# Performance work log

Hardware: AMD Instinct MI355X
Metric: run time of the kernel (lower is better)

The kernel has to match this reference:

```python
import jax, jax.numpy as jnp
import numpy as np

D_MODEL = 1024
D_STATE = 16
EPS = 1e-5


def _layernorm(x, g, b):
    mu = x.mean(-1, keepdims=True)
    xc = x - mu
    var = (xc * xc).mean(-1, keepdims=True)
    return xc * jax.lax.rsqrt(var + EPS) * g + b


def setup_inputs() -> dict:
    key = jax.random.key(0)
    ks = jax.random.split(key, 10)
    B, L, d, n = 8, 1024, D_MODEL, D_STATE
    s = 1.0 / np.sqrt(d)
    return {
        "x": jax.random.normal(ks[0], (B, L, d), jnp.float32),
        "h_prev": jnp.zeros((B, d * n), jnp.float32),
        "ln_g": jnp.ones((d,), jnp.float32),
        "ln_b": jnp.zeros((d,), jnp.float32),
        "W_ig": jax.random.uniform(ks[1], (2 * d, d), jnp.float32, -s, s),
        "W_dt": jax.random.uniform(ks[2], (d, d), jnp.float32, -s, s),
        "b_dt": jax.random.uniform(ks[3], (d,), jnp.float32, -s, s),
        "A_log": jax.random.uniform(ks[4], (d, n), jnp.float32, -3.0, -1.0),
        "W_B": jax.random.uniform(ks[5], (n, d), jnp.float32, -s, s),
        "W_C": jax.random.uniform(ks[6], (n, d), jnp.float32, -s, s),
        "D": jnp.ones((d,), jnp.float32),
        "W_out": jax.random.uniform(ks[7], (d, d), jnp.float32, -s, s),
    }


def reference(x, h_prev, ln_g, ln_b, W_ig, W_dt, b_dt, A_log, W_B, W_C, D, W_out):
    Bsz, L, d = x.shape
    n = A_log.shape[1]
    x_norm = _layernorm(x, ln_g, ln_b)
    x_proj = jnp.einsum('bld,ed->ble', x_norm, W_ig)  # [B,L,2d]
    x_in, z = x_proj[..., :d], x_proj[..., d:]
    dt = jax.nn.softplus(jnp.einsum('bld,ed->ble', x_in, W_dt) + b_dt)  # [B,L,d]
    A = -jnp.exp(A_log)  # [d,n]
    B_t = jnp.einsum('bld,nd->bln', x_in, W_B)  # [B,L,n]
    C_t = jnp.einsum('bld,nd->bln', x_in, W_C)  # [B,L,n]
    h0 = h_prev.reshape(Bsz, d, n)

    def step(h, inp):
        dt_t, xin_t, Bt_t, Ct_t = inp  # [B,d],[B,d],[B,n],[B,n]
        dA = jnp.exp(dt_t[..., None] * A)                      # [B,d,n]
        h = dA * h + (dt_t * xin_t)[..., None] * Bt_t[:, None, :]
        y_t = (h * Ct_t[:, None, :]).sum(-1)                   # [B,d]
        return h, y_t

    xs = (jnp.swapaxes(dt, 0, 1), jnp.swapaxes(x_in, 0, 1),
          jnp.swapaxes(B_t, 0, 1), jnp.swapaxes(C_t, 0, 1))
    h_final, y = jax.lax.scan(step, h0, xs)
    y = jnp.swapaxes(y, 0, 1)  # [B,L,d]
    ssm_out = y * jax.nn.silu(z) + x_in * D
    out = jnp.einsum('bld,ed->ble', ssm_out, W_out)
    return (x + out, h_final.reshape(Bsz, -1))
```

## Files before the change

### kernel.cpp

```cpp
#include <hip/hip_runtime.h>
#include <hip/hip_bf16.h>
#include <math.h>

#define DM 1024
#define NS 16
#define BSZ 8
#define LSEQ 1024
#define MROWS (BSZ*LSEQ)
#define CH 32
#define ROWP 36

typedef __bf16 bf16;
typedef bf16 bf16x8 __attribute__((ext_vector_type(8)));
typedef bf16 bf16x4 __attribute__((ext_vector_type(4)));
typedef float f32x4 __attribute__((ext_vector_type(4)));
typedef unsigned int u32;
typedef unsigned short u16;
typedef u32 u32x4 __attribute__((ext_vector_type(4)));

__device__ __forceinline__ void async16(const void* g, void* l) {
  __builtin_amdgcn_global_load_lds((const __attribute__((address_space(1))) void*)g,
                                   (__attribute__((address_space(3))) void*)l,
                                   16, 0, 0);
}

__device__ __forceinline__ float bflo(u32 u) { return __builtin_bit_cast(float, (u32)(u << 16)); }
__device__ __forceinline__ float bfhi(u32 u) { return __builtin_bit_cast(float, (u32)(u & 0xffff0000u)); }

__global__ void cast_f2b(const float* __restrict__ s, bf16* __restrict__ d, int n4) {
  int i = blockIdx.x * 256 + threadIdx.x;
  if (i < n4) {
    float4 v = ((const float4*)s)[i];
    bf16x4 o;
    o.x = (bf16)v.x; o.y = (bf16)v.y; o.z = (bf16)v.z; o.w = (bf16)v.w;
    *(bf16x4*)(d + 4 * (size_t)i) = o;
  }
}

__global__ void transpose_cast(const float* __restrict__ src, bf16* __restrict__ dst) {
  __shared__ float tile[64][65];
  const int bk = blockIdx.x * 64;
  const int bd = blockIdx.y * 64;
  const int t = threadIdx.x;
  const int c4 = t & 15;
  const int r0 = t >> 4;
#pragma unroll
  for (int p = 0; p < 4; ++p) {
    int r = r0 + p * 16;
    float4 v = *(const float4*)(src + (size_t)(bd + r) * 1024 + bk + c4 * 4);
    tile[r][c4 * 4 + 0] = v.x;
    tile[r][c4 * 4 + 1] = v.y;
    tile[r][c4 * 4 + 2] = v.z;
    tile[r][c4 * 4 + 3] = v.w;
  }
  __syncthreads();
#pragma unroll
  for (int p = 0; p < 4; ++p) {
    int r = r0 + p * 16;
    bf16x4 o;
    o.x = (bf16)tile[c4 * 4 + 0][r];
    o.y = (bf16)tile[c4 * 4 + 1][r];
    o.z = (bf16)tile[c4 * 4 + 2][r];
    o.w = (bf16)tile[c4 * 4 + 3][r];
    *(bf16x4*)(dst + (size_t)(bk + r) * 1024 + bd + c4 * 4) = o;
  }
}

__global__ void ln_kernel(const float* __restrict__ x, const float* __restrict__ g,
                          const float* __restrict__ b, bf16* __restrict__ out) {
  const size_t row = blockIdx.x;
  const int t = threadIdx.x;
  float4 v = ((const float4*)(x + row * DM))[t];
  float s = v.x + v.y + v.z + v.w;
  float s2 = v.x*v.x + v.y*v.y + v.z*v.z + v.w*v.w;
#pragma unroll
  for (int m = 1; m < 64; m <<= 1) { s += __shfl_xor(s, m, 64); s2 += __shfl_xor(s2, m, 64); }
  __shared__ float red[8];
  int wave = t >> 6, lane = t & 63;
  if (lane == 0) { red[wave] = s; red[4 + wave] = s2; }
  __syncthreads();
  s  = red[0] + red[1] + red[2] + red[3];
  s2 = red[4] + red[5] + red[6] + red[7];
  float mu  = s * (1.f / DM);
  float var = s2 * (1.f / DM) - mu * mu;
  float inv = rsqrtf(var + 1e-5f);
  float4 gg = ((const float4*)g)[t];
  float4 bb = ((const float4*)b)[t];
  bf16x4 o;
  o.x = (bf16)((v.x - mu) * inv * gg.x + bb.x);
  o.y = (bf16)((v.y - mu) * inv * gg.y + bb.y);
  o.z = (bf16)((v.z - mu) * inv * gg.z + bb.z);
  o.w = (bf16)((v.w - mu) * inv * gg.w + bb.w);
  *(bf16x4*)(out + row * DM + t * 4) = o;
}

template <int EPI, bool SWZ>
__global__ __launch_bounds__(256)
void gemm_bf16(const bf16* __restrict__ A, const bf16* __restrict__ W, int K,
               float* __restrict__ out_f, bf16* __restrict__ out_b,
               u16* __restrict__ out_u1, u16* __restrict__ out_u2,
               const float* __restrict__ aux,
               float* __restrict__ out_f3, float* __restrict__ out_f4) {
  __shared__ bf16 As[2][128 * 32];
  __shared__ bf16 Bs[2][128 * 32];
  int tx, ty;
  if (SWZ) {
    int g = blockIdx.x;
    int xcd = g & 7, slot = g >> 3;
    tx = slot >> 3;
    ty = xcd * 8 + (slot & 7);
  } else {
    tx = blockIdx.x; ty = blockIdx.y;
  }
  const int tid  = threadIdx.x;
  const int wave = tid >> 6, lane = tid & 63;
  const int lr = lane & 15, quad = lane >> 4;
  const size_t arow = (size_t)ty * 128;
  const size_t brow = (size_t)tx * 128;
  f32x4 acc[4][4] = {};

  const int srl  = lane >> 2;
  const int kg   = lane & 3;
  const int srow = wave * 32 + srl;
  const int skc  = (kg ^ ((srl >> 1) & 3)) * 8;
  const bf16* ag = A + (arow + srow) * (size_t)K + skc;
  const bf16* wg = W + (brow + srow) * (size_t)K + skc;
  bf16* asl0 = &As[0][wave * 32 * 32];
  bf16* asl1 = &As[1][wave * 32 * 32];
  bf16* bsl0 = &Bs[0][wave * 32 * 32];
  bf16* bsl1 = &Bs[1][wave * 32 * 32];

  const int rk = (quad ^ ((lr >> 1) & 3)) * 8;

  for (int k0 = 0; k0 < K; k0 += 64) {
    async16(ag + k0,                       asl0);
    async16(ag + (size_t)16 * K + k0,      asl0 + 16 * 32);
    async16(ag + k0 + 32,                  asl1);
    async16(ag + (size_t)16 * K + k0 + 32, asl1 + 16 * 32);
    async16(wg + k0,                       bsl0);
    async16(wg + (size_t)16 * K + k0,      bsl0 + 16 * 32);
    async16(wg + k0 + 32,                  bsl1);
    async16(wg + (size_t)16 * K + k0 + 32, bsl1 + 16 * 32);
    __syncthreads();
#pragma unroll
    for (int kh = 0; kh < 2; ++kh) {
      const bf16* ap = &As[kh][(((wave >> 1) * 64) + lr) * 32 + rk];
      const bf16* bp = &Bs[kh][(((wave & 1) * 64) + lr) * 32 + rk];
      bf16x8 af[4], bfr[4];
#pragma unroll
      for (int i = 0; i < 4; ++i) af[i] = *(const bf16x8*)(ap + i * 16 * 32);
#pragma unroll
      for (int j = 0; j < 4; ++j) bfr[j] = *(const bf16x8*)(bp + j * 16 * 32);
#pragma unroll
      for (int i = 0; i < 4; ++i)
#pragma unroll
        for (int j = 0; j < 4; ++j)
          acc[i][j] = __builtin_amdgcn_mfma_f32_16x16x32_bf16(af[i], bfr[j], acc[i][j], 0, 0, 0);
    }
    __syncthreads();
  }

  const size_t mbase = arow + (wave >> 1) * 64;
  const size_t nbase = brow + (wave & 1) * 64;
  if (EPI == 0) {
    if (nbase < DM) {
#pragma unroll
      for (int i = 0; i < 4; ++i)
#pragma unroll
        for (int j = 0; j < 4; ++j)
#pragma unroll
          for (int r = 0; r < 4; ++r) {
            size_t m = mbase + i * 16 + quad * 4 + r;
            size_t n = nbase + j * 16 + lr;
            out_u1[m * DM + n] = __builtin_bit_cast(u16, (bf16)acc[i][j][r]);
          }
    } else if (nbase < 2 * DM) {
#pragma unroll
      for (int i = 0; i < 4; ++i)
#pragma unroll
        for (int j = 0; j < 4; ++j)
#pragma unroll
          for (int r = 0; r < 4; ++r) {
            size_t m = mbase + i * 16 + quad * 4 + r;
            size_t n = nbase - DM + j * 16 + lr;
            out_b[m * DM + n] = (bf16)acc[i][j][r];
          }
    } else if (nbase < 3 * DM) {
#pragma unroll
      for (int i = 0; i < 4; ++i)
#pragma unroll
        for (int j = 0; j < 4; ++j)
#pragma unroll
          for (int r = 0; r < 4; ++r) {
            size_t m = mbase + i * 16 + quad * 4 + r;
            size_t n = nbase - 2 * DM + j * 16 + lr;
            float tt = acc[i][j][r] + aux[n];
            float sp = (tt > 20.f) ? tt : __logf(1.f + __expf(tt));
            out_u2[m * DM + n] = __builtin_bit_cast(u16, (bf16)sp);
          }
    } else if (nbase < 3 * DM + 2 * NS) {
#pragma unroll
      for (int i = 0; i < 4; ++i)
#pragma unroll
        for (int r = 0; r < 4; ++r) {
          size_t m = mbase + i * 16 + quad * 4 + r;
          out_f3[m * NS + lr] = acc[i][0][r];
          out_f4[m * NS + lr] = acc[i][1][r];
        }
    }
  } else {
#pragma unroll
    for (int i = 0; i < 4; ++i)
#pragma unroll
      for (int j = 0; j < 4; ++j)
#pragma unroll
        for (int r = 0; r < 4; ++r) {
          size_t m = mbase + i * 16 + quad * 4 + r;
          size_t n = nbase + j * 16 + lr;
          float v = acc[i][j][r];
          if (EPI == 2) {
            out_f[m * DM + n] = v + aux[m * DM + n];
          } else {
            out_b[m * (size_t)DM + n] = (bf16)v;
          }
        }
  }
}

__global__ __launch_bounds__(256)
void scan_kernel(const u16* __restrict__ dt_b, const u16* __restrict__ xi_b,
                 const bf16* __restrict__ z_b,
                 const float* __restrict__ B_t, const float* __restrict__ C_t,
                 const float* __restrict__ A_log, const float* __restrict__ h_prev,
                 const float* __restrict__ Dvec,
                 bf16* __restrict__ ssm_out, float* __restrict__ h_final) {
  const int blk = blockIdx.x;
  const int b = blk >> 6;
  const int d0 = (blk & 63) * 16;
  const int t = threadIdx.x;
  const int n = t & 15, dl = t >> 4;
  const int d = d0 + dl;
  const float Ac2 = -__expf(A_log[d * NS + n]) * 1.44269504f;
  float h = h_prev[(size_t)b * DM * NS + (size_t)d * NS + n];

  __shared__ u32   dxs[2][16][ROWP];
  __shared__ float Bsh[2][16][ROWP];
  __shared__ float Csh[2][16][ROWP];
  __shared__ float ys_p[CH][16][17];

  const size_t base_row = (size_t)b * LSEQ;
  const int l_a = t >> 4, c_a = t & 15;
  const float Dva = Dvec[d0 + c_a];

  {
    size_t ga = (base_row + l_a) * DM + d0 + c_a;
    size_t gb = (base_row + l_a + 16) * DM + d0 + c_a;
    dxs[0][c_a][l_a]      = (u32)dt_b[ga] | ((u32)xi_b[ga] << 16);
    dxs[0][c_a][l_a + 16] = (u32)dt_b[gb] | ((u32)xi_b[gb] << 16);
    size_t gB = base_row * NS;
    Bsh[0][c_a][l_a]      = B_t[gB + t];
    Csh[0][c_a][l_a]      = C_t[gB + t];
    Bsh[0][c_a][l_a + 16] = B_t[gB + t + 256];
    Csh[0][c_a][l_a + 16] = C_t[gB + t + 256];
  }
  float za = (float)z_b[(base_row + l_a) * DM + d0 + c_a];
  float zb = (float)z_b[(base_row + l_a + 16) * DM + d0 + c_a];
  __syncthreads();

  for (int c = 0; c < LSEQ / CH; ++c) {
    const int cur = c & 1, nxt = cur ^ 1;
    u32 pdxa, pdxb; float pBa, pBb, pCa, pCb, pza, pzb;
    if (c + 1 < LSEQ / CH) {
      size_t l0 = (size_t)(c + 1) * CH;
      size_t ga = (base_row + l0 + l_a) * DM + d0 + c_a;
      size_t gb = (base_row + l0 + l_a + 16) * DM + d0 + c_a;
      pdxa = (u32)dt_b[ga] | ((u32)xi_b[ga] << 16);
      pdxb = (u32)dt_b[gb] | ((u32)xi_b[gb] << 16);
      pza = (float)z_b[ga]; pzb = (float)z_b[gb];
      size_t gB = (base_row + l0) * NS;
      pBa = B_t[gB + t];       pCa = C_t[gB + t];
      pBb = B_t[gB + t + 256]; pCb = C_t[gB + t + 256];
    }
#pragma unroll
    for (int l4 = 0; l4 < CH; l4 += 4) {
      u32x4 dx4 = *(const u32x4*)&dxs[cur][dl][l4];
      f32x4 b4  = *(const f32x4*)&Bsh[cur][n][l4];
      f32x4 c4  = *(const f32x4*)&Csh[cur][n][l4];
#pragma unroll
      for (int i = 0; i < 4; ++i) {
        float dtv = bflo(dx4[i]), xiv = bfhi(dx4[i]);
        float a = __builtin_amdgcn_exp2f(dtv * Ac2);
        h = fmaf(a, h, (dtv * xiv) * b4[i]);
        ys_p[l4 + i][dl][n] = h * c4[i];
      }
    }
    __syncthreads();
    {
      float s1 = 0.f, s2 = 0.f;
#pragma unroll
      for (int k = 0; k < 16; ++k) {
        s1 += ys_p[l_a][c_a][k];
        s2 += ys_p[l_a + 16][c_a][k];
      }
      float x1 = bfhi(dxs[cur][c_a][l_a]);
      float x2 = bfhi(dxs[cur][c_a][l_a + 16]);
      float g1 = za / (1.f + __expf(-za));
      float g2 = zb / (1.f + __expf(-zb));
      size_t l0 = (size_t)c * CH;
      ssm_out[(base_row + l0 + l_a) * DM + d0 + c_a]      = (bf16)(s1 * g1 + x1 * Dva);
      ssm_out[(base_row + l0 + l_a + 16) * DM + d0 + c_a] = (bf16)(s2 * g2 + x2 * Dva);
    }
    if (c + 1 < LSEQ / CH) {
      dxs[nxt][c_a][l_a]      = pdxa;
      dxs[nxt][c_a][l_a + 16] = pdxb;
      Bsh[nxt][c_a][l_a]      = pBa;
      Csh[nxt][c_a][l_a]      = pCa;
      Bsh[nxt][c_a][l_a + 16] = pBb;
      Csh[nxt][c_a][l_a + 16] = pCb;
      za = pza; zb = pzb;
    }
    __syncthreads();
  }
  h_final[(size_t)b * DM * NS + (size_t)d0 * NS + t] = h;
}

extern "C" void kernel_launch(void* const* d_in, const int* in_sizes, int n_in,
                              void* d_out, int out_size, void* d_ws, size_t ws_size,
                              hipStream_t stream) {
  const float* x      = (const float*)d_in[0];
  const float* h_prev = (const float*)d_in[1];
  const float* ln_g   = (const float*)d_in[2];
  const float* ln_b   = (const float*)d_in[3];
  const float* W_ig   = (const float*)d_in[4];
  const float* W_dt   = (const float*)d_in[5];
  const float* b_dt   = (const float*)d_in[6];
  const float* A_log  = (const float*)d_in[7];
  const float* W_B    = (const float*)d_in[8];
  const float* W_C    = (const float*)d_in[9];
  const float* Dvec   = (const float*)d_in[10];
  const float* W_out  = (const float*)d_in[11];

  char* ws = (char*)d_ws;
  size_t off = 0;
  auto alloc = [&](size_t bytes) -> char* {
    char* p = ws + off;
    off += (bytes + 255) & ~(size_t)255;
    return p;
  };
  bf16*  wmega_b = (bf16*)alloc((size_t)3200 * DM * 2);
  bf16*  wstack_b= (bf16*)alloc((size_t)1152 * DM * 2);
  bf16*  wigT_b  = (bf16*)alloc((size_t)DM * DM * 2);
  bf16*  wout_b  = (bf16*)alloc((size_t)DM * DM * 2);
  bf16*  xnorm_b = (bf16*)alloc((size_t)MROWS * DM * 2);
  u16*   xi_w    = (u16*)alloc((size_t)MROWS * DM * 2);
  u16*   dt_w    = (u16*)alloc((size_t)MROWS * DM * 2);
  bf16*  z_bb    = (bf16*)alloc((size_t)MROWS * DM * 2);
  bf16*  ssm_b   = (bf16*)alloc((size_t)MROWS * DM * 2);
  float* Bt      = (float*)alloc((size_t)MROWS * NS * 4);
  float* Ct      = (float*)alloc((size_t)MROWS * NS * 4);
  (void)ws_size; (void)in_sizes; (void)n_in; (void)out_size;

  float* out_main = (float*)d_out;
  float* out_h    = (float*)d_out + (size_t)MROWS * DM;

  cast_f2b<<<(2 * DM * DM / 4 + 255) / 256, 256, 0, stream>>>(W_ig, wmega_b, 2 * DM * DM / 4);
  cast_f2b<<<(DM * DM / 4 + 255) / 256, 256, 0, stream>>>(W_dt, wstack_b, DM * DM / 4);
  cast_f2b<<<(NS * DM / 4 + 255) / 256, 256, 0, stream>>>(W_B, wstack_b + (size_t)DM * DM, NS * DM / 4);
  cast_f2b<<<(NS * DM / 4 + 255) / 256, 256, 0, stream>>>(W_C, wstack_b + (size_t)(DM + NS) * DM, NS * DM / 4);
  cast_f2b<<<(DM * DM / 4 + 255) / 256, 256, 0, stream>>>(W_out, wout_b, DM * DM / 4);
  transpose_cast<<<dim3(16, 16), 256, 0, stream>>>(W_ig, wigT_b);

  ln_kernel<<<MROWS, 256, 0, stream>>>(x, ln_g, ln_b, xnorm_b);

  gemm_bf16<3, false><<<dim3(8, 9), 256, 0, stream>>>(wstack_b, wigT_b, DM,
      nullptr, wmega_b + (size_t)2048 * DM, nullptr, nullptr, nullptr, nullptr, nullptr);

  gemm_bf16<0, true><<<1600, 256, 0, stream>>>(xnorm_b, wmega_b, DM,
      nullptr, z_bb, xi_w, dt_w, b_dt, Bt, Ct);

  scan_kernel<<<512, 256, 0, stream>>>(dt_w, xi_w, z_bb, Bt, Ct, A_log, h_prev,
                                       Dvec, ssm_b, out_h);

  gemm_bf16<2, true><<<512, 256, 0, stream>>>(ssm_b, wout_b, DM,
      out_main, nullptr, nullptr, nullptr, x, nullptr, nullptr);
}
```

Before: 345.3 us.

## Double-buffer GEMM K-loop so async LDS loads overlap MFMA compute

Restructures the GEMM main loop into a ping-pong pipeline. Each 32-wide K half-tile is prefetched into one LDS buffer with async global-to-LDS loads while the MFMAs run on the other buffer. The goal is to hide global load latency that was previously exposed before every compute phase. Barriers per iteration stay at two, and correctness relies on the async loads having completed by the time each barrier is passed.

After: 358.3 us. 3.8% more time.

```diff
diff --git a/kernel.cpp b/kernel.cpp
--- a/kernel.cpp
+++ b/kernel.cpp
@@ -125,38 +125,44 @@
   const int skc  = (kg ^ ((srl >> 1) & 3)) * 8;
   const bf16* ag = A + (arow + srow) * (size_t)K + skc;
   const bf16* wg = W + (brow + srow) * (size_t)K + skc;
-  bf16* asl0 = &As[0][wave * 32 * 32];
-  bf16* asl1 = &As[1][wave * 32 * 32];
-  bf16* bsl0 = &Bs[0][wave * 32 * 32];
-  bf16* bsl1 = &Bs[1][wave * 32 * 32];
+  bf16* a_dst0 = &As[0][wave * 32 * 32];
+  bf16* a_dst1 = &As[1][wave * 32 * 32];
+  bf16* b_dst0 = &Bs[0][wave * 32 * 32];
+  bf16* b_dst1 = &Bs[1][wave * 32 * 32];
 
   const int rk = (quad ^ ((lr >> 1) & 3)) * 8;
-
+  const bf16* ap0 = &As[0][(((wave >> 1) * 64) + lr) * 32 + rk];
+  const bf16* bp0 = &Bs[0][(((wave & 1) * 64) + lr) * 32 + rk];
+  const bf16* ap1 = &As[1][(((wave >> 1) * 64) + lr) * 32 + rk];
+  const bf16* bp1 = &Bs[1][(((wave & 1) * 64) + lr) * 32 + rk];
+
+  auto STAGE = [&](bf16* adst, bf16* bdst, int kk) {
+    async16(ag + kk,                       adst);
+    async16(ag + (size_t)16 * K + kk,      adst + 16 * 32);
+    async16(wg + kk,                       bdst);
+    async16(wg + (size_t)16 * K + kk,      bdst + 16 * 32);
+  };
+  auto COMPUTE = [&](const bf16* ap, const bf16* bp) {
+    bf16x8 af[4], bfr[4];
+#pragma unroll
+    for (int i = 0; i < 4; ++i) af[i] = *(const bf16x8*)(ap + i * 16 * 32);
+#pragma unroll
+    for (int j = 0; j < 4; ++j) bfr[j] = *(const bf16x8*)(bp + j * 16 * 32);
+#pragma unroll
+    for (int i = 0; i < 4; ++i)
+#pragma unroll
+      for (int j = 0; j < 4; ++j)
+        acc[i][j] = __builtin_amdgcn_mfma_f32_16x16x32_bf16(af[i], bfr[j], acc[i][j], 0, 0, 0);
+  };
+
+  STAGE(a_dst0, b_dst0, 0);
+  __syncthreads();
   for (int k0 = 0; k0 < K; k0 += 64) {
-    async16(ag + k0,                       asl0);
-    async16(ag + (size_t)16 * K + k0,      asl0 + 16 * 32);
-    async16(ag + k0 + 32,                  asl1);
-    async16(ag + (size_t)16 * K + k0 + 32, asl1 + 16 * 32);
-    async16(wg + k0,                       bsl0);
-    async16(wg + (size_t)16 * K + k0,      bsl0 + 16 * 32);
-    async16(wg + k0 + 32,                  bsl1);
-    async16(wg + (size_t)16 * K + k0 + 32, bsl1 + 16 * 32);
+    STAGE(a_dst1, b_dst1, k0 + 32);
+    COMPUTE(ap0, bp0);
     __syncthreads();
-#pragma unroll
-    for (int kh = 0; kh < 2; ++kh) {
-      const bf16* ap = &As[kh][(((wave >> 1) * 64) + lr) * 32 + rk];
-      const bf16* bp = &Bs[kh][(((wave & 1) * 64) + lr) * 32 + rk];
-      bf16x8 af[4], bfr[4];
-#pragma unroll
-      for (int i = 0; i < 4; ++i) af[i] = *(const bf16x8*)(ap + i * 16 * 32);
-#pragma unroll
-      for (int j = 0; j < 4; ++j) bfr[j] = *(const bf16x8*)(bp + j * 16 * 32);
-#pragma unroll
-      for (int i = 0; i < 4; ++i)
-#pragma unroll
-        for (int j = 0; j < 4; ++j)
-          acc[i][j] = __builtin_amdgcn_mfma_f32_16x16x32_bf16(af[i], bfr[j], acc[i][j], 0, 0, 0);
-    }
+    if (k0 + 64 < K) STAGE(a_dst0, b_dst0, k0 + 64);
+    COMPUTE(ap1, bp1);
     __syncthreads();
   }
 
```
